# Performance work log

Measured on AMD Instinct MI355X. Metric: run time of the kernel, lower is better.

The kernel has to match this reference:

```python
import jax, jax.numpy as jnp
import numpy as np

B, N, K = 8, 2048, 64
RADII = (0.1, 0.3, 0.7)
TU = 256   # t_net_units
U = 512    # mmtsc_units
BLK = [(512, 512), (512, 256), (256, 170)]  # pce_depth=3, filters U//(i+1)
EPS = 1e-3  # keras BatchNormalization epsilon
BN_SCALE = np.float32(1.0 / np.sqrt(1.0 + EPS))  # inference BN: mean=0, var=1


def bn(x, g, b):
    return x * (g * BN_SCALE) + b


def setup_inputs():
    key = jax.random.key(0)
    ks = jax.random.split(key, 32)
    r = lambda i, sh, s=0.1: jax.random.normal(ks[i], sh, dtype=jnp.float32) * s
    inp = {
        "points": jax.random.normal(ks[0], (B, N, 3), dtype=jnp.float32),
        "noise": jax.random.uniform(ks[1], (B, N, N), dtype=jnp.float32),
        "tw": r(2, (3, TU)), "tb": r(3, (TU,)),
        "tg1": 1.0 + r(4, (TU,)), "tbt1": r(5, (TU,)),
        "td1w": r(6, (TU, TU)), "td1b": r(7, (TU,)),
        "tg2": 1.0 + r(8, (TU,)), "tbt2": r(9, (TU,)),
        "td2w": r(10, (TU, 9), 0.01), "td2b": jnp.ones((9,), jnp.float32),
        "c1w": r(11, (3 * K * 3, U)), "c1b": r(12, (U,)),
        "g1": 1.0 + r(13, (U,)), "be1": r(14, (U,)),
        "rw": r(15, (U, U)), "rb": r(16, (U,)),
    }
    for i, (ci, co) in enumerate(BLK):
        j = 17 + 4 * i
        inp[f"b{i+1}w"] = r(j, (ci, co))
        inp[f"b{i+1}b"] = r(j + 1, (co,))
        inp[f"b{i+1}g"] = 1.0 + r(j + 2, (co,))
        inp[f"b{i+1}be"] = r(j + 3, (co,))
    return inp


def reference(points, noise, tw, tb, tg1, tbt1, td1w, td1b, tg2, tbt2, td2w, td2b,
              c1w, c1b, g1, be1, rw, rb,
              b1w, b1b, b1g, b1be, b2w, b2b, b2g, b2be, b3w, b3b, b3g, b3be):
    relu = jax.nn.relu
    # ---- T-Net (dropout inactive at inference) ----
    x = relu(bn(points @ tw + tb, tg1, tbt1))       # [B,N,TU] (1x1 conv)
    x = jnp.max(x, axis=1)                          # GlobalMaxPooling1D -> [B,TU]
    x = relu(bn(x @ td1w + td1b, tg2, tbt2))        # [B,TU]
    T = (x @ td2w + td2b).reshape(-1, 3, 3)         # [B,3,3]
    pts = points @ T                                # [B,N,3]
    # ---- pairwise distances + multi-scale ball query ----
    diff = pts[:, :, None, :] - pts[:, None, :, :]  # [B,N,N,3]
    d = jax.lax.stop_gradient(jnp.sqrt(jnp.sum(diff * diff, axis=-1)))  # [B,N,N]
    bidx = jnp.arange(B)[:, None, None]
    groups = []
    for rad in RADII:
        score = jnp.where(d <= rad, noise, 0.0)     # mask * uniform
        idx = jnp.argsort(-score, axis=-1)[:, :, :K]  # descending, top-K  [B,N,K]
        groups.append(pts[bidx, idx])               # gather -> [B,N,K,3]
    feats = jnp.concatenate(groups, axis=-1).reshape(B, N, 3 * K * 3)  # [B,N,576]
    # ---- MLP stack (1x1 convs) ----
    f = relu(bn(feats @ c1w + c1b, g1, be1))        # [B,N,U]
    f = f + (f @ rw + rb)                           # residual
    for w, b_, g, be in ((b1w, b1b, b1g, b1be), (b2w, b2b, b2g, b2be), (b3w, b3b, b3g, b3be)):
        f = relu(bn(f @ w + b_, g, be))
    return jnp.max(f, axis=1)                       # [B,170]
```

## Files before the change

### kernel.cpp

```cpp
#include <hip/hip_runtime.h>
#include <hip/hip_bf16.h>


#define BN_SCALE 0.99950037468777f

typedef short short8 __attribute__((ext_vector_type(8)));
typedef short sh4 __attribute__((ext_vector_type(4)));
typedef float floatx4 __attribute__((ext_vector_type(4)));

__device__ inline short f2bf(float x) {
    __hip_bfloat16 h = __float2bfloat16(x);
    return *reinterpret_cast<short*>(&h);
}
__device__ inline float bf2f(short s) {
    return __uint_as_float(((unsigned)(unsigned short)s) << 16);
}

#define OFF_FEATS 0
#define OFF_W     18874368
#define OFF_C1WT  (OFF_W)
#define OFF_RWT   (OFF_C1WT + 589824)
#define OFF_B1WT  (OFF_RWT + 524288)
#define OFF_B2WT  (OFF_B1WT + 524288)
#define OFF_B3WT  (OFF_B2WT + 262144)
#define OFF_PTS   (OFF_B3WT + 131072)
#define OFF_PART  (OFF_PTS + 196608)

__global__ __launch_bounds__(256)
void init_k(const float* __restrict__ c1w, const float* __restrict__ rw,
            const float* __restrict__ b1w, const float* __restrict__ b2w,
            const float* __restrict__ b3w,
            short* __restrict__ c1wT, short* __restrict__ rwT,
            short* __restrict__ b1wT, short* __restrict__ b2wT,
            short* __restrict__ b3wT,
            const float* __restrict__ points, const float* __restrict__ tw,
            const float* __restrict__ tb, const float* __restrict__ tg1,
            const float* __restrict__ tbt1, float* __restrict__ part,
            float* __restrict__ outF, int out_n) {
    __shared__ float smem[64 * 65];
    const int bid = blockIdx.x;
    if (bid < 248) {
        float (*tile)[65] = (float(*)[65])smem;
        const float* src; short* dst; int K, N, t;
        if (bid < 72)       { src = c1w; dst = c1wT; K = 576; N = 512; t = bid; }
        else if (bid < 136) { src = rw;  dst = rwT;  K = 512; N = 512; t = bid - 72; }
        else if (bid < 200) { src = b1w; dst = b1wT; K = 512; N = 512; t = bid - 136; }
        else if (bid < 232) { src = b2w; dst = b2wT; K = 512; N = 256; t = bid - 200; }
        else                { src = b3w; dst = b3wT; K = 256; N = 170; t = bid - 232; }
        int ktiles = K >> 6;
        int k0 = (t % ktiles) * 64, n0 = (t / ktiles) * 64;
        int tx = threadIdx.x & 63, ty = threadIdx.x >> 6;
#pragma unroll
        for (int p = 0; p < 16; p++) {
            int r = p * 4 + ty;
            int n = n0 + tx;
            tile[r][tx] = (n < N) ? src[(size_t)(k0 + r) * N + n] : 0.f;
        }
        __syncthreads();
#pragma unroll
        for (int p = 0; p < 16; p++) {
            int r = p * 4 + ty;
            dst[(size_t)(n0 + r) * K + k0 + tx] = f2bf(tile[tx][r]);
        }
    } else if (bid < 312) {
        float* spts = smem;
        const int t2 = bid - 248;
        const int chunk = t2 & 7, b = t2 >> 3;
        const int u = threadIdx.x;
        const float* pb = points + ((size_t)b * 2048 + chunk * 256) * 3;
        for (int i = u; i < 768; i += 256) spts[i] = pb[i];
        const float w0 = tw[u], w1 = tw[256 + u], w2 = tw[512 + u];
        const float bi = tb[u];
        const float gs = tg1[u] * BN_SCALE, bt = tbt1[u];
        __syncthreads();
        float m = 0.f;
        for (int nn = 0; nn < 256; nn++) {
            float v = spts[nn * 3] * w0 + spts[nn * 3 + 1] * w1 +
                      spts[nn * 3 + 2] * w2 + bi;
            v = fmaxf(v * gs + bt, 0.f);
            m = fmaxf(m, v);
        }
        part[((b * 8 + chunk) << 8) + u] = m;
    } else {
        for (int i = threadIdx.x; i < out_n; i += 256) outF[i] = 0.f;
    }
}

__global__ __launch_bounds__(1024)
void tnet2_k(const float* __restrict__ points, const float* __restrict__ part,
             const float* __restrict__ td1w, const float* __restrict__ td1b,
             const float* __restrict__ tg2, const float* __restrict__ tbt2,
             const float* __restrict__ td2w, const float* __restrict__ td2b,
             float* __restrict__ pts_out) {
    __shared__ float sx[256], sp[4][256], sx2[256], sp2[9][32], sT[9];
    const int b = blockIdx.x;
    const int tid = threadIdx.x;
    if (tid < 256) {
        float m = 0.f;
#pragma unroll
        for (int c = 0; c < 8; c++) m = fmaxf(m, part[((b * 8 + c) << 8) + tid]);
        sx[tid] = m;
    }
    __syncthreads();
    {
        int t = tid & 255, g = tid >> 8;
        float s = 0.f;
#pragma unroll 8
        for (int i = 0; i < 64; i++) {
            int v = g * 64 + i;
            s += sx[v] * td1w[v * 256 + t];
        }
        sp[g][t] = s;
    }
    __syncthreads();
    if (tid < 256) {
        float s = td1b[tid] + sp[0][tid] + sp[1][tid] + sp[2][tid] + sp[3][tid];
        sx2[tid] = fmaxf(s * (tg2[tid] * BN_SCALE) + tbt2[tid], 0.f);
    }
    __syncthreads();
    if (tid < 288) {
        int j = tid / 32, vg = tid & 31;
        float s = 0.f;
#pragma unroll
        for (int i = 0; i < 8; i++) {
            int v = vg * 8 + i;
            s += sx2[v] * td2w[v * 9 + j];
        }
        sp2[j][vg] = s;
    }
    __syncthreads();
    if (tid < 9) {
        float s = td2b[tid];
        for (int vg = 0; vg < 32; vg++) s += sp2[tid][vg];
        sT[tid] = s;
    }
    __syncthreads();
    for (int n = tid; n < 2048; n += 1024) {
        size_t idx = ((size_t)b * 2048 + n) * 3;
        float p0 = points[idx], p1 = points[idx + 1], p2 = points[idx + 2];
        pts_out[idx]     = p0 * sT[0] + p1 * sT[3] + p2 * sT[6];
        pts_out[idx + 1] = p0 * sT[1] + p1 * sT[4] + p2 * sT[7];
        pts_out[idx + 2] = p0 * sT[2] + p1 * sT[5] + p2 * sT[8];
    }
}

__device__ inline unsigned dpp_shr1(unsigned v) {
    return (unsigned)__builtin_amdgcn_update_dpp(0, (int)v, 0x138 ,
                                                 0xF, 0xF, false);
}

__device__ inline void ins_one(unsigned& llo, unsigned& lhi, unsigned vlo,
                               unsigned vhi, int lane) {
    unsigned long long lv = ((unsigned long long)lhi << 32) | llo;
    unsigned long long vv = ((unsigned long long)vhi << 32) | vlo;
    unsigned long long ltm = __ballot(lv < vv);
    if (ltm) {
        int p = __builtin_ctzll(ltm);
        unsigned uplo = dpp_shr1(llo);
        unsigned uphi = dpp_shr1(lhi);
        if (lane >= p) {
            llo = (lane == p) ? vlo : uplo;
            lhi = (lane == p) ? vhi : uphi;
        }
    }
}

__device__ inline void run_q(unsigned& llo, unsigned& lhi, unsigned long long& th,
                             unsigned klo, unsigned khi, unsigned long long qual,
                             int lane) {
    do {
        int src = __builtin_ctzll(qual);
        qual &= qual - 1;
        unsigned vlo = (unsigned)__builtin_amdgcn_readlane((int)klo, src);
        unsigned vhi = (unsigned)__builtin_amdgcn_readlane((int)khi, src);
        ins_one(llo, lhi, vlo, vhi, lane);
    } while (qual);
    th = ((unsigned long long)(unsigned)__builtin_amdgcn_readlane((int)lhi, 63) << 32)
         | (unsigned)__builtin_amdgcn_readlane((int)llo, 63);
}

__device__ inline void init_radius(bool in, unsigned nb, unsigned klo, int lane,
                                   unsigned& llo, unsigned& lhi,
                                   unsigned long long& th) {
    unsigned long long inm = __ballot(in);
    int S = 64 - __builtin_popcountll(inm);
    int mbI = __builtin_amdgcn_mbcnt_hi((unsigned)(inm >> 32),
              __builtin_amdgcn_mbcnt_lo((unsigned)inm, 0));
    int mbS = lane - mbI;
    int dst = in ? (S + mbI) : mbS;
    llo = (unsigned)__builtin_amdgcn_ds_permute(dst << 2, in ? 0 : (int)klo);
    lhi = 0;
    if (inm) {
        do {
            int src = __builtin_ctzll(inm);
            inm &= inm - 1;
            unsigned vlo = (unsigned)__builtin_amdgcn_readlane((int)klo, src);
            unsigned vhi = (unsigned)__builtin_amdgcn_readlane((int)nb, src);
            ins_one(llo, lhi, vlo, vhi, lane);
        } while (inm);
    }
    th = ((unsigned long long)(unsigned)__builtin_amdgcn_readlane((int)lhi, 63) << 32)
         | (unsigned)__builtin_amdgcn_readlane((int)llo, 63);
}

__global__ __launch_bounds__(512)
void topk_feats_k(const float* __restrict__ pts, const float* __restrict__ noise,
                  short* __restrict__ feats) {
    __shared__ float sxp[2048], syp[2048], szp[2048];
    const int b = blockIdx.y;
    const int tid = threadIdx.x;
    const int lane = tid & 63;
    const int wave = tid >> 6;
    const int n = blockIdx.x * 8 + wave;
    const float* nrow = noise + ((size_t)b * 2048 + n) * 2048;
    float ncur = nrow[lane];
    float nnxt = nrow[64 + lane];
    for (int i = tid; i < 2048; i += 512) {
        size_t p = ((size_t)b * 2048 + i) * 3;
        sxp[i] = pts[p];
        syp[i] = pts[p + 1];
        szp[i] = pts[p + 2];
    }
    __syncthreads();
    const float qx = sxp[n], qy = syp[n], qz = szp[n];

    unsigned L0lo, L0hi, L1lo, L1hi, L2lo, L2hi;
    unsigned long long th0, th1, th2;
    {
        float dx = qx - sxp[lane], dy = qy - syp[lane], dz = qz - szp[lane];
        float d = sqrtf(dx * dx + dy * dy + dz * dz);
        unsigned nb = __float_as_uint(ncur);
        unsigned klo = 2047 - lane;
        init_radius(d <= 0.1f, nb, klo, lane, L0lo, L0hi, th0);
        init_radius(d <= 0.3f, nb, klo, lane, L1lo, L1hi, th1);
        init_radius(d <= 0.7f, nb, klo, lane, L2lo, L2hi, th2);
    }
    for (int base = 64; base < 2048; base += 64) {
        float cur = nnxt;
        if (base + 64 < 2048) nnxt = nrow[base + 64 + lane];
        const int j = base + lane;
        float dx = qx - sxp[j], dy = qy - syp[j], dz = qz - szp[j];
        float d = sqrtf(dx * dx + dy * dy + dz * dz);
        unsigned nb = __float_as_uint(cur);
        unsigned klo = 2047 - j;
        unsigned k0hi = (d <= 0.1f) ? nb : 0u;
        unsigned k1hi = (d <= 0.3f) ? nb : 0u;
        unsigned k2hi = (d <= 0.7f) ? nb : 0u;
        unsigned long long key0 = ((unsigned long long)k0hi << 32) | klo;
        unsigned long long key1 = ((unsigned long long)k1hi << 32) | klo;
        unsigned long long key2 = ((unsigned long long)k2hi << 32) | klo;
        unsigned long long q0 = __ballot(key0 > th0);
        unsigned long long q1 = __ballot(key1 > th1);
        unsigned long long q2 = __ballot(key2 > th2);
        if (q0) run_q(L0lo, L0hi, th0, klo, k0hi, q0, lane);
        if (q1) run_q(L1lo, L1hi, th1, klo, k1hi, q1, lane);
        if (q2) run_q(L2lo, L2hi, th2, klo, k2hi, q2, lane);
    }
    size_t basef = ((size_t)b * 2048 + n) * 576 + (size_t)lane * 9;
    int j0 = 2047 - (int)(L0lo & 0x7FFu);
    int j1 = 2047 - (int)(L1lo & 0x7FFu);
    int j2 = 2047 - (int)(L2lo & 0x7FFu);
    feats[basef + 0] = f2bf(sxp[j0]);
    feats[basef + 1] = f2bf(syp[j0]);
    feats[basef + 2] = f2bf(szp[j0]);
    feats[basef + 3] = f2bf(sxp[j1]);
    feats[basef + 4] = f2bf(syp[j1]);
    feats[basef + 5] = f2bf(szp[j1]);
    feats[basef + 6] = f2bf(sxp[j2]);
    feats[basef + 7] = f2bf(syp[j2]);
    feats[basef + 8] = f2bf(szp[j2]);
}

template <int NF, int EPI, int BSRC, int K>
__device__ __forceinline__ void layer(
    const short* __restrict__ WT, const short* __restrict__ gfeats,
    const short* actIn, short* actOut,
    const float* __restrict__ bias, const float* __restrict__ gamma,
    const float* __restrict__ beta, float* __restrict__ outF,
    int m0, int Nact) {
    const int tid = threadIdx.x;
    const int lane = tid & 63;
    const int wave = tid >> 6;
    const int lr = lane & 15, lq = lane >> 4;
    const int n0w = wave * (NF * 16);

    floatx4 acc[NF][4];
#pragma unroll
    for (int i = 0; i < NF; i++)
#pragma unroll
        for (int j = 0; j < 4; j++) acc[i][j] = (floatx4){0.f, 0.f, 0.f, 0.f};

#pragma unroll 2
    for (int k0 = 0; k0 < K; k0 += 32) {
        short8 af[NF], bf[4];
#pragma unroll
        for (int i = 0; i < NF; i++)
            af[i] = *(const short8*)(WT + (size_t)(n0w + i * 16 + lr) * K + k0 + lq * 8);
        if (BSRC == 0) {
#pragma unroll
            for (int j = 0; j < 4; j++)
                bf[j] = *(const short8*)(gfeats + (size_t)(m0 + j * 16 + lr) * 576 + k0 + lq * 8);
        } else {
#pragma unroll
            for (int j = 0; j < 4; j++) {
                int m = j * 16 + lr;
                bf[j] = *(const short8*)((const char*)actIn + m * 1024 +
                                         ((k0 * 2 + lq * 16) ^ ((m & 7) << 4)));
            }
        }
#pragma unroll
        for (int i = 0; i < NF; i++)
#pragma unroll
            for (int j = 0; j < 4; j++)
                acc[i][j] = __builtin_amdgcn_mfma_f32_16x16x32_bf16(af[i], bf[j],
                                                                    acc[i][j], 0, 0, 0);
    }

    if (EPI == 2) {
        const int bb = m0 >> 11;
#pragma unroll
        for (int i = 0; i < NF; i++) {
            int nb = n0w + i * 16 + lq * 4;
            float bi[4], gs[4], bt[4], cm[4];
#pragma unroll
            for (int rg = 0; rg < 4; rg++) {
                int n = nb + rg;
                bool ok = n < Nact;
                bi[rg] = ok ? bias[n] : 0.f;
                gs[rg] = ok ? gamma[n] * BN_SCALE : 0.f;
                bt[rg] = ok ? beta[n] : 0.f;
                cm[rg] = 0.f;
            }
#pragma unroll
            for (int j = 0; j < 4; j++)
#pragma unroll
                for (int rg = 0; rg < 4; rg++) {
                    float v = fmaxf((acc[i][j][rg] + bi[rg]) * gs[rg] + bt[rg], 0.f);
                    cm[rg] = fmaxf(cm[rg], v);
                }
#pragma unroll
            for (int rg = 0; rg < 4; rg++) {
                cm[rg] = fmaxf(cm[rg], __shfl_xor(cm[rg], 1));
                cm[rg] = fmaxf(cm[rg], __shfl_xor(cm[rg], 2));
                cm[rg] = fmaxf(cm[rg], __shfl_xor(cm[rg], 4));
                cm[rg] = fmaxf(cm[rg], __shfl_xor(cm[rg], 8));
            }
            if (lr == 0) {
#pragma unroll
                for (int rg = 0; rg < 4; rg++) {
                    int n = nb + rg;
                    if (n < Nact)
                        atomicMax((unsigned*)&outF[bb * 170 + n],
                                  __float_as_uint(cm[rg]));
                }
            }
        }
    } else {
#pragma unroll
        for (int i = 0; i < NF; i++) {
            int nb = n0w + i * 16 + lq * 4;
            floatx4 bi = *(const floatx4*)(bias + nb);
            floatx4 gs = {0.f, 0.f, 0.f, 0.f}, bt = {0.f, 0.f, 0.f, 0.f};
            if (EPI == 0) {
                gs = *(const floatx4*)(gamma + nb);
                bt = *(const floatx4*)(beta + nb);
            }
#pragma unroll
            for (int j = 0; j < 4; j++) {
                int m = j * 16 + lr;
                int off = m * 1024 + ((nb * 2) ^ ((m & 7) << 4));
                sh4 pk;
                if (EPI == 1) {
                    sh4 rs = *(const sh4*)((const char*)actIn + off);
#pragma unroll
                    for (int rg = 0; rg < 4; rg++)
                        pk[rg] = f2bf(acc[i][j][rg] + bi[rg] + bf2f(rs[rg]));
                } else {
#pragma unroll
                    for (int rg = 0; rg < 4; rg++)
                        pk[rg] = f2bf(fmaxf((acc[i][j][rg] + bi[rg]) *
                                            (gs[rg] * BN_SCALE) + bt[rg], 0.f));
                }
                *(sh4*)((char*)actOut + off) = pk;
            }
        }
    }
}

__global__ __launch_bounds__(256, 1)
void mlp_k(const short* __restrict__ feats,
           const short* __restrict__ c1wT, const short* __restrict__ rwT,
           const short* __restrict__ b1wT, const short* __restrict__ b2wT,
           const short* __restrict__ b3wT,
           const float* __restrict__ c1b, const float* __restrict__ g1,
           const float* __restrict__ be1, const float* __restrict__ rb,
           const float* __restrict__ b1b, const float* __restrict__ b1g,
           const float* __restrict__ b1be,
           const float* __restrict__ b2b, const float* __restrict__ b2g,
           const float* __restrict__ b2be,
           const float* __restrict__ b3b, const float* __restrict__ b3g,
           const float* __restrict__ b3be, float* __restrict__ outF) {
    __shared__ __align__(16) short actA[64 * 512];
    __shared__ __align__(16) short actB[64 * 512];
    const int m0 = blockIdx.x * 64;

    layer<8, 0, 0, 576>(c1wT, feats, nullptr, actA, c1b, g1, be1, nullptr, m0, 512);
    __syncthreads();
    layer<8, 1, 1, 512>(rwT, nullptr, actA, actB, rb, nullptr, nullptr, nullptr, m0, 512);
    __syncthreads();
    layer<8, 0, 1, 512>(b1wT, nullptr, actB, actA, b1b, b1g, b1be, nullptr, m0, 512);
    __syncthreads();
    layer<4, 0, 1, 512>(b2wT, nullptr, actA, actB, b2b, b2g, b2be, nullptr, m0, 256);
    __syncthreads();
    layer<4, 2, 1, 256>(b3wT, nullptr, actB, nullptr, b3b, b3g, b3be, outF, m0, 170);
}

extern "C" void kernel_launch(void* const* d_in, const int* in_sizes, int n_in,
                              void* d_out, int out_size, void* d_ws, size_t ws_size,
                              hipStream_t stream) {
    const float* points = (const float*)d_in[0];
    const float* noise  = (const float*)d_in[1];
    const float* tw   = (const float*)d_in[2];
    const float* tb   = (const float*)d_in[3];
    const float* tg1  = (const float*)d_in[4];
    const float* tbt1 = (const float*)d_in[5];
    const float* td1w = (const float*)d_in[6];
    const float* td1b = (const float*)d_in[7];
    const float* tg2  = (const float*)d_in[8];
    const float* tbt2 = (const float*)d_in[9];
    const float* td2w = (const float*)d_in[10];
    const float* td2b = (const float*)d_in[11];
    const float* c1w  = (const float*)d_in[12];
    const float* c1b  = (const float*)d_in[13];
    const float* g1   = (const float*)d_in[14];
    const float* be1  = (const float*)d_in[15];
    const float* rw   = (const float*)d_in[16];
    const float* rb   = (const float*)d_in[17];
    const float* b1w  = (const float*)d_in[18];
    const float* b1b  = (const float*)d_in[19];
    const float* b1g  = (const float*)d_in[20];
    const float* b1be = (const float*)d_in[21];
    const float* b2w  = (const float*)d_in[22];
    const float* b2b  = (const float*)d_in[23];
    const float* b2g  = (const float*)d_in[24];
    const float* b2be = (const float*)d_in[25];
    const float* b3w  = (const float*)d_in[26];
    const float* b3b  = (const float*)d_in[27];
    const float* b3g  = (const float*)d_in[28];
    const float* b3be = (const float*)d_in[29];

    char* ws = (char*)d_ws;
    short* feats = (short*)(ws + OFF_FEATS);
    short* c1wT  = (short*)(ws + OFF_C1WT);
    short* rwT   = (short*)(ws + OFF_RWT);
    short* b1wT  = (short*)(ws + OFF_B1WT);
    short* b2wT  = (short*)(ws + OFF_B2WT);
    short* b3wT  = (short*)(ws + OFF_B3WT);
    float* pts   = (float*)(ws + OFF_PTS);
    float* part  = (float*)(ws + OFF_PART);
    float* outF  = (float*)d_out;

    init_k<<<313, 256, 0, stream>>>(c1w, rw, b1w, b2w, b3w,
                                    c1wT, rwT, b1wT, b2wT, b3wT,
                                    points, tw, tb, tg1, tbt1, part,
                                    outF, out_size);
    tnet2_k<<<8, 1024, 0, stream>>>(points, part, td1w, td1b, tg2, tbt2,
                                    td2w, td2b, pts);
    topk_feats_k<<<dim3(256, 8), 512, 0, stream>>>(pts, noise, feats);
    mlp_k<<<256, 256, 0, stream>>>(feats, c1wT, rwT, b1wT, b2wT, b3wT,
                                   c1b, g1, be1, rb, b1b, b1g, b1be,
                                   b2b, b2g, b2be, b3b, b3g, b3be, outF);
}
```

Measured before the change: 450.4 us.

## Use single in-place LDS activation buffer in MLP and fuse T-Net stages

The MLP kernel now keeps one 64KB shared activation buffer instead of two. Each layer writes its output back in place after a barrier, with the residual inputs read into registers first. Halving LDS use and raising launch bounds to 2 blocks per CU is meant to let two workgroups share a CU. Separately, the T-Net point-conv max pass moves out of init_k into a fused single-block-per-batch kernel that keeps the points in LDS, which removes the partial-max buffer. This adds a barrier per layer and leaves only 8 blocks to do the T-Net first stage.

```diff
diff --git a/kernel.cpp b/kernel.cpp
--- a/kernel.cpp
+++ b/kernel.cpp
@@ -24,7 +24,6 @@
 #define OFF_B2WT  (OFF_B1WT + 524288)
 #define OFF_B3WT  (OFF_B2WT + 262144)
 #define OFF_PTS   (OFF_B3WT + 131072)
-#define OFF_PART  (OFF_PTS + 196608)
 
 __global__ __launch_bounds__(256)
 void init_k(const float* __restrict__ c1w, const float* __restrict__ rw,
@@ -33,14 +32,10 @@
             short* __restrict__ c1wT, short* __restrict__ rwT,
             short* __restrict__ b1wT, short* __restrict__ b2wT,
             short* __restrict__ b3wT,
-            const float* __restrict__ points, const float* __restrict__ tw,
-            const float* __restrict__ tb, const float* __restrict__ tg1,
-            const float* __restrict__ tbt1, float* __restrict__ part,
             float* __restrict__ outF, int out_n) {
-    __shared__ float smem[64 * 65];
+    __shared__ float tile[64][65];
     const int bid = blockIdx.x;
     if (bid < 248) {
-        float (*tile)[65] = (float(*)[65])smem;
         const float* src; short* dst; int K, N, t;
         if (bid < 72)       { src = c1w; dst = c1wT; K = 576; N = 512; t = bid; }
         else if (bid < 136) { src = rw;  dst = rwT;  K = 512; N = 512; t = bid - 72; }
@@ -62,45 +57,44 @@
             int r = p * 4 + ty;
             dst[(size_t)(n0 + r) * K + k0 + tx] = f2bf(tile[tx][r]);
         }
-    } else if (bid < 312) {
-        float* spts = smem;
-        const int t2 = bid - 248;
-        const int chunk = t2 & 7, b = t2 >> 3;
-        const int u = threadIdx.x;
-        const float* pb = points + ((size_t)b * 2048 + chunk * 256) * 3;
-        for (int i = u; i < 768; i += 256) spts[i] = pb[i];
+    } else {
+        for (int i = threadIdx.x; i < out_n; i += 256) outF[i] = 0.f;
+    }
+}
+
+__global__ __launch_bounds__(1024)
+void tnet12_k(const float* __restrict__ points,
+              const float* __restrict__ tw, const float* __restrict__ tb,
+              const float* __restrict__ tg1, const float* __restrict__ tbt1,
+              const float* __restrict__ td1w, const float* __restrict__ td1b,
+              const float* __restrict__ tg2, const float* __restrict__ tbt2,
+              const float* __restrict__ td2w, const float* __restrict__ td2b,
+              float* __restrict__ pts_out) {
+    __shared__ float spts[2048 * 3];
+    __shared__ float sx[256], sp[4][256], sx2[256], sp2[9][32], sT[9];
+    const int b = blockIdx.x;
+    const int tid = threadIdx.x;
+    const float* pb = points + (size_t)b * 2048 * 3;
+    for (int i = tid; i < 6144; i += 1024) spts[i] = pb[i];
+    __syncthreads();
+    {
+        int u = tid & 255, c = tid >> 8;
         const float w0 = tw[u], w1 = tw[256 + u], w2 = tw[512 + u];
         const float bi = tb[u];
         const float gs = tg1[u] * BN_SCALE, bt = tbt1[u];
-        __syncthreads();
+        const float* spc = spts + c * 512 * 3;
         float m = 0.f;
-        for (int nn = 0; nn < 256; nn++) {
-            float v = spts[nn * 3] * w0 + spts[nn * 3 + 1] * w1 +
-                      spts[nn * 3 + 2] * w2 + bi;
-            v = fmaxf(v * gs + bt, 0.f);
-            m = fmaxf(m, v);
-        }
-        part[((b * 8 + chunk) << 8) + u] = m;
-    } else {
-        for (int i = threadIdx.x; i < out_n; i += 256) outF[i] = 0.f;
-    }
-}
-
-__global__ __launch_bounds__(1024)
-void tnet2_k(const float* __restrict__ points, const float* __restrict__ part,
-             const float* __restrict__ td1w, const float* __restrict__ td1b,
-             const float* __restrict__ tg2, const float* __restrict__ tbt2,
-             const float* __restrict__ td2w, const float* __restrict__ td2b,
-             float* __restrict__ pts_out) {
-    __shared__ float sx[256], sp[4][256], sx2[256], sp2[9][32], sT[9];
-    const int b = blockIdx.x;
-    const int tid = threadIdx.x;
-    if (tid < 256) {
-        float m = 0.f;
-#pragma unroll
-        for (int c = 0; c < 8; c++) m = fmaxf(m, part[((b * 8 + c) << 8) + tid]);
-        sx[tid] = m;
-    }
+        for (int nn = 0; nn < 512; nn++) {
+            float v = spc[nn * 3] * w0 + spc[nn * 3 + 1] * w1 +
+                      spc[nn * 3 + 2] * w2 + bi;
+            m = fmaxf(m, fmaxf(v * gs + bt, 0.f));
+        }
+        sp[c][u] = m;
+    }
+    __syncthreads();
+    if (tid < 256)
+        sx[tid] = fmaxf(fmaxf(sp[0][tid], sp[1][tid]),
+                        fmaxf(sp[2][tid], sp[3][tid]));
     __syncthreads();
     {
         int t = tid & 255, g = tid >> 8;
@@ -136,8 +130,8 @@
     }
     __syncthreads();
     for (int n = tid; n < 2048; n += 1024) {
+        float p0 = spts[n * 3], p1 = spts[n * 3 + 1], p2 = spts[n * 3 + 2];
         size_t idx = ((size_t)b * 2048 + n) * 3;
-        float p0 = points[idx], p1 = points[idx + 1], p2 = points[idx + 2];
         pts_out[idx]     = p0 * sT[0] + p1 * sT[3] + p2 * sT[6];
         pts_out[idx + 1] = p0 * sT[1] + p1 * sT[4] + p2 * sT[7];
         pts_out[idx + 2] = p0 * sT[2] + p1 * sT[5] + p2 * sT[8];
@@ -274,7 +268,7 @@
 template <int NF, int EPI, int BSRC, int K>
 __device__ __forceinline__ void layer(
     const short* __restrict__ WT, const short* __restrict__ gfeats,
-    const short* actIn, short* actOut,
+    short* actS,
     const float* __restrict__ bias, const float* __restrict__ gamma,
     const float* __restrict__ beta, float* __restrict__ outF,
     int m0, int Nact) {
@@ -304,7 +298,7 @@
 #pragma unroll
             for (int j = 0; j < 4; j++) {
                 int m = j * 16 + lr;
-                bf[j] = *(const short8*)((const char*)actIn + m * 1024 +
+                bf[j] = *(const short8*)((const char*)actS + m * 1024 +
                                          ((k0 * 2 + lq * 16) ^ ((m & 7) << 4)));
             }
         }
@@ -355,39 +349,54 @@
                 }
             }
         }
-    } else {
+        return;
+    }
+
+    sh4 rs[NF][4];
+    if (EPI == 1) {
 #pragma unroll
         for (int i = 0; i < NF; i++) {
             int nb = n0w + i * 16 + lq * 4;
-            floatx4 bi = *(const floatx4*)(bias + nb);
-            floatx4 gs = {0.f, 0.f, 0.f, 0.f}, bt = {0.f, 0.f, 0.f, 0.f};
-            if (EPI == 0) {
-                gs = *(const floatx4*)(gamma + nb);
-                bt = *(const floatx4*)(beta + nb);
-            }
 #pragma unroll
             for (int j = 0; j < 4; j++) {
                 int m = j * 16 + lr;
-                int off = m * 1024 + ((nb * 2) ^ ((m & 7) << 4));
-                sh4 pk;
-                if (EPI == 1) {
-                    sh4 rs = *(const sh4*)((const char*)actIn + off);
-#pragma unroll
-                    for (int rg = 0; rg < 4; rg++)
-                        pk[rg] = f2bf(acc[i][j][rg] + bi[rg] + bf2f(rs[rg]));
-                } else {
-#pragma unroll
-                    for (int rg = 0; rg < 4; rg++)
-                        pk[rg] = f2bf(fmaxf((acc[i][j][rg] + bi[rg]) *
-                                            (gs[rg] * BN_SCALE) + bt[rg], 0.f));
-                }
-                *(sh4*)((char*)actOut + off) = pk;
-            }
-        }
-    }
-}
-
-__global__ __launch_bounds__(256, 1)
+                rs[i][j] = *(const sh4*)((const char*)actS +
+                                         m * 1024 + ((nb * 2) ^ ((m & 7) << 4)));
+            }
+        }
+    }
+    __syncthreads();
+
+#pragma unroll
+    for (int i = 0; i < NF; i++) {
+        int nb = n0w + i * 16 + lq * 4;
+        floatx4 bi = *(const floatx4*)(bias + nb);
+        floatx4 gs = {0.f, 0.f, 0.f, 0.f}, bt = {0.f, 0.f, 0.f, 0.f};
+        if (EPI == 0) {
+            gs = *(const floatx4*)(gamma + nb);
+            bt = *(const floatx4*)(beta + nb);
+        }
+#pragma unroll
+        for (int j = 0; j < 4; j++) {
+            int m = j * 16 + lr;
+            int off = m * 1024 + ((nb * 2) ^ ((m & 7) << 4));
+            sh4 pk;
+            if (EPI == 1) {
+#pragma unroll
+                for (int rg = 0; rg < 4; rg++)
+                    pk[rg] = f2bf(acc[i][j][rg] + bi[rg] + bf2f(rs[i][j][rg]));
+            } else {
+#pragma unroll
+                for (int rg = 0; rg < 4; rg++)
+                    pk[rg] = f2bf(fmaxf((acc[i][j][rg] + bi[rg]) *
+                                        (gs[rg] * BN_SCALE) + bt[rg], 0.f));
+            }
+            *(sh4*)((char*)actS + off) = pk;
+        }
+    }
+}
+
+__global__ __launch_bounds__(256, 2)
 void mlp_k(const short* __restrict__ feats,
            const short* __restrict__ c1wT, const short* __restrict__ rwT,
            const short* __restrict__ b1wT, const short* __restrict__ b2wT,
@@ -400,19 +409,18 @@
            const float* __restrict__ b2be,
            const float* __restrict__ b3b, const float* __restrict__ b3g,
            const float* __restrict__ b3be, float* __restrict__ outF) {
-    __shared__ __align__(16) short actA[64 * 512];
-    __shared__ __align__(16) short actB[64 * 512];
+    __shared__ __align__(16) short actS[64 * 512];
     const int m0 = blockIdx.x * 64;
 
-    layer<8, 0, 0, 576>(c1wT, feats, nullptr, actA, c1b, g1, be1, nullptr, m0, 512);
-    __syncthreads();
-    layer<8, 1, 1, 512>(rwT, nullptr, actA, actB, rb, nullptr, nullptr, nullptr, m0, 512);
-    __syncthreads();
-    layer<8, 0, 1, 512>(b1wT, nullptr, actB, actA, b1b, b1g, b1be, nullptr, m0, 512);
-    __syncthreads();
-    layer<4, 0, 1, 512>(b2wT, nullptr, actA, actB, b2b, b2g, b2be, nullptr, m0, 256);
-    __syncthreads();
-    layer<4, 2, 1, 256>(b3wT, nullptr, actB, nullptr, b3b, b3g, b3be, outF, m0, 170);
+    layer<8, 0, 0, 576>(c1wT, feats, actS, c1b, g1, be1, nullptr, m0, 512);
+    __syncthreads();
+    layer<8, 1, 1, 512>(rwT, nullptr, actS, rb, nullptr, nullptr, nullptr, m0, 512);
+    __syncthreads();
+    layer<8, 0, 1, 512>(b1wT, nullptr, actS, b1b, b1g, b1be, nullptr, m0, 512);
+    __syncthreads();
+    layer<4, 0, 1, 512>(b2wT, nullptr, actS, b2b, b2g, b2be, nullptr, m0, 256);
+    __syncthreads();
+    layer<4, 2, 1, 256>(b3wT, nullptr, actS, b3b, b3g, b3be, outF, m0, 170);
 }
 
 extern "C" void kernel_launch(void* const* d_in, const int* in_sizes, int n_in,
@@ -457,15 +465,13 @@
     short* b2wT  = (short*)(ws + OFF_B2WT);
     short* b3wT  = (short*)(ws + OFF_B3WT);
     float* pts   = (float*)(ws + OFF_PTS);
-    float* part  = (float*)(ws + OFF_PART);
     float* outF  = (float*)d_out;
 
-    init_k<<<313, 256, 0, stream>>>(c1w, rw, b1w, b2w, b3w,
+    init_k<<<249, 256, 0, stream>>>(c1w, rw, b1w, b2w, b3w,
                                     c1wT, rwT, b1wT, b2wT, b3wT,
-                                    points, tw, tb, tg1, tbt1, part,
                                     outF, out_size);
-    tnet2_k<<<8, 1024, 0, stream>>>(points, part, td1w, td1b, tg2, tbt2,
-                                    td2w, td2b, pts);
+    tnet12_k<<<8, 1024, 0, stream>>>(points, tw, tb, tg1, tbt1,
+                                     td1w, td1b, tg2, tbt2, td2w, td2b, pts);
     topk_feats_k<<<dim3(256, 8), 512, 0, stream>>>(pts, noise, feats);
     mlp_k<<<256, 256, 0, stream>>>(feats, c1wT, rwT, b1wT, b2wT, b3wT,
                                    c1b, g1, be1, rb, b1b, b1g, b1be,
```

After: 475.6 us. 1.06x slower.
